# Optimization experiments

Hardware: AMD Instinct MI355X
Metric: run time of the kernel (lower is better)

## Reference

```python
import jax, jax.numpy as jnp
import numpy as np

N_NODES = 100000
N_EDGES = 3200000
IN_CH = 384
HID = 128

def _gcn_layer(x, src, dst, norm, W, b, n_nodes):
    # PyG GCNConv: h = x @ W; out[dst] += norm * h[src]; out += b
    h = x @ W                                   # [N, out_ch]
    msg = h[src] * norm[:, None]                 # [E+N, out_ch] gather + scale
    out = jax.ops.segment_sum(msg, dst, num_segments=n_nodes)
    return out + b

def setup_inputs() -> dict:
    key = jax.random.key(0)
    k = jax.random.split(key, 7)
    x = jax.random.normal(k[0], (N_NODES, IN_CH), dtype=jnp.float32)
    edge_index = jax.random.randint(k[1], (2, N_EDGES), 0, N_NODES, dtype=jnp.int64)
    # Glorot-style init for GCN weights, zeros for biases (PyG default)
    W1 = jax.random.normal(k[2], (IN_CH, HID), dtype=jnp.float32) / np.sqrt(IN_CH)
    b1 = jnp.zeros((HID,), dtype=jnp.float32)
    W2 = jax.random.normal(k[3], (HID, HID), dtype=jnp.float32) / np.sqrt(HID)
    b2 = jnp.zeros((HID,), dtype=jnp.float32)
    return {"x": x, "edge_index": edge_index, "W1": W1, "b1": b1, "W2": W2, "b2": b2}

def reference(x, edge_index, W1, b1, W2, b2):
    n_nodes = x.shape[0]
    # GCNConv default: add self-loops, symmetric normalization D^-1/2 A D^-1/2
    loop = jnp.arange(n_nodes, dtype=edge_index.dtype)
    src = jnp.concatenate([edge_index[0], loop])   # [E+N]
    dst = jnp.concatenate([edge_index[1], loop])   # [E+N]
    deg = jax.ops.segment_sum(jnp.ones_like(dst, dtype=x.dtype), dst, num_segments=n_nodes)
    deg_inv_sqrt = jnp.where(deg > 0, jax.lax.rsqrt(jnp.maximum(deg, 1.0)), 0.0)
    norm = deg_inv_sqrt[src] * deg_inv_sqrt[dst]   # [E+N]
    h = _gcn_layer(x, src, dst, norm, W1, b1, n_nodes)
    h = jax.nn.relu(h)                              # dropout is identity in eval mode
    out = _gcn_layer(h, src, dst, norm, W2, b2, n_nodes)
    return out
```

## Files before the change

kernel.cpp:

```cpp
#include <hip/hip_runtime.h>

#define N_NODES 100000
#define N_EDGES 3200000
#define IN_CH   384
#define HID     128
#define BKT_SHIFT 7
#define NBKT ((N_NODES + 127) >> 7)
#define NTILE 8
#define TILE_SZ 12500
#define NBINS (NBKT * NTILE)
#define BINBLK 128
#define BTHREADS 512
#define CHUNK4 (N_EDGES / 4 / BINBLK)
#define GS_NBLK ((NBINS + 1023) / 1024)

typedef __attribute__((ext_vector_type(8))) short          bf16x8;
typedef __attribute__((ext_vector_type(8))) unsigned short u16x8;
typedef __attribute__((ext_vector_type(4))) float          f32x4;

static __device__ __forceinline__ unsigned short f2bf(float f) {
    unsigned u = __float_as_uint(f);
    unsigned r = (u + 0x7fffu + ((u >> 16) & 1u)) >> 16;
    return (unsigned short)r;
}

__global__ void k_wt2(const float* __restrict__ W1, const float* __restrict__ W2,
                      unsigned short* __restrict__ wt1, unsigned short* __restrict__ wt2) {
    int i = blockIdx.x * blockDim.x + threadIdx.x;
    if (i < IN_CH * 128) {
        int k = i >> 7, n = i & 127;
        wt1[(size_t)n * IN_CH + k] = f2bf(W1[i]);
    } else if (i < (IN_CH + HID) * 128) {
        int j = i - IN_CH * 128;
        int k = j >> 7, n = j & 127;
        wt2[(size_t)n * HID + k] = f2bf(W2[j]);
    }
}

__global__ __launch_bounds__(BTHREADS) void k_bhist2(const int* __restrict__ src,
                                                     const int* __restrict__ dst,
                                                     unsigned* __restrict__ hist) {
    __shared__ unsigned lh[NBINS];
    for (int i = threadIdx.x; i < NBINS; i += BTHREADS) lh[i] = 0;
    __syncthreads();
    const int4* s4 = (const int4*)src;
    const int4* d4 = (const int4*)dst;
    const int base = blockIdx.x * CHUNK4;
    for (int i = threadIdx.x; i < CHUNK4; i += BTHREADS) {
        int4 sv = s4[base + i];
        int4 dv = d4[base + i];
        atomicAdd(&lh[(dv.x >> BKT_SHIFT) * NTILE + (unsigned)sv.x / TILE_SZ], 1u);
        atomicAdd(&lh[(dv.y >> BKT_SHIFT) * NTILE + (unsigned)sv.y / TILE_SZ], 1u);
        atomicAdd(&lh[(dv.z >> BKT_SHIFT) * NTILE + (unsigned)sv.z / TILE_SZ], 1u);
        atomicAdd(&lh[(dv.w >> BKT_SHIFT) * NTILE + (unsigned)sv.w / TILE_SZ], 1u);
    }
    __syncthreads();
    for (int i = threadIdx.x; i < NBINS; i += BTHREADS) hist[i * BINBLK + blockIdx.x] = lh[i];
}

__global__ __launch_bounds__(BINBLK) void k_bscan(unsigned* __restrict__ hist,
                                                  unsigned* __restrict__ bintot) {
    __shared__ unsigned s[BINBLK];
    const int b = blockIdx.x, t = threadIdx.x;
    unsigned v = hist[b * BINBLK + t];
    s[t] = v;
    __syncthreads();
    for (int off = 1; off < BINBLK; off <<= 1) {
        unsigned x = s[t];
        unsigned y = (t >= off) ? s[t - off] : 0u;
        __syncthreads();
        s[t] = x + y;
        __syncthreads();
    }
    hist[b * BINBLK + t] = s[t] - v;
    if (t == BINBLK - 1) bintot[b] = s[BINBLK - 1];
}

__global__ __launch_bounds__(1024) void gs1(const unsigned* __restrict__ in,
                                            unsigned* __restrict__ out,
                                            unsigned* __restrict__ bsum, int n) {
    __shared__ unsigned s[1024];
    const int t = threadIdx.x;
    const int i = blockIdx.x * 1024 + t;
    unsigned v = (i < n) ? in[i] : 0u;
    s[t] = v;
    __syncthreads();
    for (int off = 1; off < 1024; off <<= 1) {
        unsigned x = s[t];
        unsigned y = (t >= off) ? s[t - off] : 0u;
        __syncthreads();
        s[t] = x + y;
        __syncthreads();
    }
    if (i < n) out[i] = s[t] - v;
    if (t == 1023) bsum[blockIdx.x] = s[1023];
}

__global__ void gs2(unsigned* __restrict__ bsum, int nb) {
    if (threadIdx.x == 0 && blockIdx.x == 0) {
        unsigned run = 0;
        for (int i = 0; i < nb; i++) { unsigned v = bsum[i]; bsum[i] = run; run += v; }
    }
}

__global__ __launch_bounds__(1024) void gs3(unsigned* __restrict__ out,
                                            const unsigned* __restrict__ bsum, int n, int total) {
    const int i = blockIdx.x * 1024 + threadIdx.x;
    if (i < n) out[i] += bsum[blockIdx.x];
    if (i == 0) out[n] = (unsigned)total;
}

__global__ __launch_bounds__(BTHREADS) void k_bscat2(const int* __restrict__ src,
                                                     const int* __restrict__ dst,
                                                     const unsigned* __restrict__ hist,
                                                     const unsigned* __restrict__ B2,
                                                     unsigned* __restrict__ ebuf) {
    __shared__ unsigned lcur[NBINS];
    for (int i = threadIdx.x; i < NBINS; i += BTHREADS)
        lcur[i] = B2[i] + hist[i * BINBLK + blockIdx.x];
    __syncthreads();
    const int4* s4 = (const int4*)src;
    const int4* d4 = (const int4*)dst;
    const int base = blockIdx.x * CHUNK4;
    for (int i = threadIdx.x; i < CHUNK4; i += BTHREADS) {
        int4 sv = s4[base + i];
        int4 dv = d4[base + i];
        unsigned p;
        p = atomicAdd(&lcur[(dv.x >> BKT_SHIFT) * NTILE + (unsigned)sv.x / TILE_SZ], 1u);
        ebuf[p] = ((unsigned)(dv.x & 127) << 17) | (unsigned)sv.x;
        p = atomicAdd(&lcur[(dv.y >> BKT_SHIFT) * NTILE + (unsigned)sv.y / TILE_SZ], 1u);
        ebuf[p] = ((unsigned)(dv.y & 127) << 17) | (unsigned)sv.y;
        p = atomicAdd(&lcur[(dv.z >> BKT_SHIFT) * NTILE + (unsigned)sv.z / TILE_SZ], 1u);
        ebuf[p] = ((unsigned)(dv.z & 127) << 17) | (unsigned)sv.z;
        p = atomicAdd(&lcur[(dv.w >> BKT_SHIFT) * NTILE + (unsigned)sv.w / TILE_SZ], 1u);
        ebuf[p] = ((unsigned)(dv.w & 127) << 17) | (unsigned)sv.w;
    }
}

__global__ __launch_bounds__(BTHREADS) void k_fill5(const unsigned* __restrict__ ebuf,
                                                    const unsigned* __restrict__ B2,
                                                    unsigned* __restrict__ rowptr,
                                                    float* __restrict__ dis,
                                                    int* __restrict__ csr, int N, int E) {
    __shared__ unsigned lcnt[128];
    __shared__ unsigned lcur[128];
    const int b = blockIdx.x, t = threadIdx.x;
    const int n0 = b << BKT_SHIFT;
    const int cnt = min(128, N - n0);
    if (t < 128) lcnt[t] = 0;
    __syncthreads();
    const unsigned beg = B2[b * NTILE], end = B2[b * NTILE + NTILE];
    for (unsigned i = beg + t; i < end; i += BTHREADS)
        atomicAdd(&lcnt[ebuf[i] >> 17], 1u);
    __syncthreads();
    unsigned deg_t = (t < 128) ? lcnt[t] : 0u;
    if (t < 128) lcur[t] = deg_t;
    __syncthreads();
    for (int off = 1; off < 128; off <<= 1) {
        unsigned x = 0;
        if (t < 128) {
            x = lcur[t];
            if (t >= off) x += lcur[t - off];
        }
        __syncthreads();
        if (t < 128) lcur[t] = x;
        __syncthreads();
    }
    if (t < cnt) {
        unsigned ex = beg + lcur[t] - deg_t;
        rowptr[n0 + t] = ex;
        dis[n0 + t] = rsqrtf((float)(deg_t + 1u));
        lcur[t] = ex;
    }
    if (b == (int)gridDim.x - 1 && t == 0) rowptr[N] = (unsigned)E;
    __syncthreads();
    for (unsigned i = beg + t; i < end; i += BTHREADS) {
        unsigned v = ebuf[i];
        unsigned pos = atomicAdd(&lcur[v >> 17], 1u);
        csr[pos] = (int)(v & 0x1FFFFu);
    }
}

template<bool AF32>
__global__ __launch_bounds__(256) void k_gemm_mfma(const void* __restrict__ Ap,
                                                   const unsigned short* __restrict__ Wt,
                                                   const float* __restrict__ dis,
                                                   unsigned short* __restrict__ C,
                                                   int M, int K) {
    __shared__ unsigned short As[128][40];
    __shared__ unsigned short Bs[128][40];
    const int tid = threadIdx.x;
    const int w = tid >> 6;
    const int l = tid & 63;
    const int row0 = blockIdx.x * 128;

    f32x4 acc[2][8];
#pragma unroll
    for (int i = 0; i < 2; i++)
#pragma unroll
        for (int f = 0; f < 8; f++) acc[i][f] = (f32x4){0.f, 0.f, 0.f, 0.f};

    for (int k0 = 0; k0 < K; k0 += 32) {
#pragma unroll
        for (int t = 0; t < 2; t++) {
            int g = tid + t * 256;
            int r = g >> 2, k8 = (g & 3) * 8;
            int ar = row0 + r;
            u16x8 u = {0, 0, 0, 0, 0, 0, 0, 0};
            if (AF32) {
                if (ar < M) {
                    const float* ap = (const float*)Ap + (size_t)ar * K + k0 + k8;
                    float4 v0 = *(const float4*)ap;
                    float4 v1 = *(const float4*)(ap + 4);
                    u[0] = f2bf(v0.x); u[1] = f2bf(v0.y); u[2] = f2bf(v0.z); u[3] = f2bf(v0.w);
                    u[4] = f2bf(v1.x); u[5] = f2bf(v1.y); u[6] = f2bf(v1.z); u[7] = f2bf(v1.w);
                }
            } else {
                if (ar < M)
                    u = *(const u16x8*)((const unsigned short*)Ap + (size_t)ar * K + k0 + k8);
            }
            *(u16x8*)&As[r][k8] = u;
        }
#pragma unroll
        for (int t = 0; t < 2; t++) {
            int g = tid + t * 256;
            int n = g >> 2, k8 = (g & 3) * 8;
            *(u16x8*)&Bs[n][k8] = *(const u16x8*)&Wt[(size_t)n * K + k0 + k8];
        }
        __syncthreads();

        bf16x8 a0 = *(const bf16x8*)&As[w * 32 + (l & 15)][(l >> 4) * 8];
        bf16x8 a1 = *(const bf16x8*)&As[w * 32 + 16 + (l & 15)][(l >> 4) * 8];
#pragma unroll
        for (int f = 0; f < 8; f++) {
            bf16x8 bfr = *(const bf16x8*)&Bs[f * 16 + (l & 15)][(l >> 4) * 8];
            acc[0][f] = __builtin_amdgcn_mfma_f32_16x16x32_bf16(a0, bfr, acc[0][f], 0, 0, 0);
            acc[1][f] = __builtin_amdgcn_mfma_f32_16x16x32_bf16(a1, bfr, acc[1][f], 0, 0, 0);
        }
        __syncthreads();
    }

    const int colb = l & 15;
    const int rowq = (l >> 4) * 4;
#pragma unroll
    for (int i = 0; i < 2; i++)
#pragma unroll
        for (int r = 0; r < 4; r++) {
            int row = row0 + w * 32 + i * 16 + rowq + r;
            if (row < M) {
                float dv = dis[row];
#pragma unroll
                for (int f = 0; f < 8; f++)
                    C[(size_t)row * 128 + f * 16 + colb] = f2bf(dv * acc[i][f][r]);
            }
        }
}

template<int RELU, int OUTBF>
__global__ __launch_bounds__(256) void k_aggregate(const unsigned short* __restrict__ h,
                                                   const int* __restrict__ csr_src,
                                                   const unsigned* __restrict__ rowptr,
                                                   const float* __restrict__ dis,
                                                   const float* __restrict__ bias,
                                                   void* __restrict__ outp, int N) {
    const int wid = (int)((blockIdx.x * (blockDim.x >> 6)) + (threadIdx.x >> 6));
    const int d = __builtin_amdgcn_readfirstlane(wid);
    if (d >= N) return;
    const int lane = threadIdx.x & 63;
    const unsigned beg = rowptr[d], end = rowptr[d + 1];
    const float dd = dis[d];
    const unsigned* h1 = reinterpret_cast<const unsigned*>(h);

    unsigned hv = h1[(size_t)d * 64 + lane];
    float ax = __uint_as_float(hv << 16);
    float ay = __uint_as_float(hv & 0xffff0000u);

    unsigned e = beg;
    for (; e + 8 <= end; e += 8) {
        int s[8];
        unsigned v[8];
#pragma unroll
        for (int u = 0; u < 8; u++) s[u] = csr_src[e + u];
#pragma unroll
        for (int u = 0; u < 8; u++) v[u] = h1[(size_t)s[u] * 64 + lane];
#pragma unroll
        for (int u = 0; u < 8; u++) {
            ax += __uint_as_float(v[u] << 16);
            ay += __uint_as_float(v[u] & 0xffff0000u);
        }
    }
    for (; e < end; e++) {
        int s0 = csr_src[e];
        unsigned v0 = h1[(size_t)s0 * 64 + lane];
        ax += __uint_as_float(v0 << 16);
        ay += __uint_as_float(v0 & 0xffff0000u);
    }
    float2 bv = reinterpret_cast<const float2*>(bias)[lane];
    float r0 = fmaf(dd, ax, bv.x);
    float r1 = fmaf(dd, ay, bv.y);
    if (RELU) { r0 = fmaxf(r0, 0.f); r1 = fmaxf(r1, 0.f); }
    if (OUTBF) {
        unsigned pack = (unsigned)f2bf(r0) | ((unsigned)f2bf(r1) << 16);
        reinterpret_cast<unsigned*>(outp)[(size_t)d * 64 + lane] = pack;
    } else {
        reinterpret_cast<float2*>(outp)[(size_t)d * 64 + lane] = make_float2(r0, r1);
    }
}

extern "C" void kernel_launch(void* const* d_in, const int* in_sizes, int n_in,
                              void* d_out, int out_size, void* d_ws, size_t ws_size,
                              hipStream_t stream) {
    const float* x  = (const float*)d_in[0];
    const int*   ei = (const int*)d_in[1];
    const float* W1 = (const float*)d_in[2];
    const float* b1 = (const float*)d_in[3];
    const float* W2 = (const float*)d_in[4];
    const float* b2 = (const float*)d_in[5];
    const int* src = ei;
    const int* dst = ei + N_EDGES;
    float* out = (float*)d_out;

    char* ws = (char*)d_ws;
    float*          dis    = (float*)ws;
    unsigned*       rowptr = (unsigned*)(ws + 400128);
    unsigned*       B2     = (unsigned*)(ws + 800256);
    unsigned*       bintot = (unsigned*)(ws + 825344);
    unsigned*       gsb    = (unsigned*)(ws + 850432);
    unsigned short* wt1    = (unsigned short*)(ws + 850688);
    unsigned short* wt2    = (unsigned short*)(ws + 948992);
    unsigned*       hist   = (unsigned*)(ws + 981760);
    unsigned*       ebuf   = (unsigned*)(ws + 4184832);
    int*            csr    = (int*)(ws + 16984832);
    unsigned short* hbf    = (unsigned short*)(ws + 29784832);
    unsigned short* abf    = (unsigned short*)(ws + 55384832);

    k_wt2<<<((IN_CH + HID) * 128 + 255) / 256, 256, 0, stream>>>(W1, W2, wt1, wt2);

    k_bhist2<<<BINBLK, BTHREADS, 0, stream>>>(src, dst, hist);
    k_bscan<<<NBINS, BINBLK, 0, stream>>>(hist, bintot);
    gs1<<<GS_NBLK, 1024, 0, stream>>>(bintot, B2, gsb, NBINS);
    gs2<<<1, 64, 0, stream>>>(gsb, GS_NBLK);
    gs3<<<GS_NBLK, 1024, 0, stream>>>(B2, gsb, NBINS, N_EDGES);
    k_bscat2<<<BINBLK, BTHREADS, 0, stream>>>(src, dst, hist, B2, ebuf);
    k_fill5<<<NBKT, BTHREADS, 0, stream>>>(ebuf, B2, rowptr, dis, csr, N_NODES, N_EDGES);

    k_gemm_mfma<true><<<(N_NODES + 127) / 128, 256, 0, stream>>>(x, wt1, dis, hbf, N_NODES, IN_CH);
    k_aggregate<1, 1><<<(N_NODES * 64 + 255) / 256, 256, 0, stream>>>(hbf, csr, rowptr, dis, b1, abf, N_NODES);

    k_gemm_mfma<false><<<(N_NODES + 127) / 128, 256, 0, stream>>>(abf, wt2, dis, hbf, N_NODES, HID);
    k_aggregate<0, 0><<<(N_NODES * 64 + 255) / 256, 256, 0, stream>>>(hbf, csr, rowptr, dis, b2, out, N_NODES);
}
```

Before: 399.4 us.

## Double binning blocks and fuse three-pass global scan into one block

Raises the number of histogram/scatter blocks from 128 to 256 so the edge binning kernels spread across more CUs, and enlarges the hist buffer, shifting later workspace offsets. Replaces the three-kernel global prefix scan (block scan, serial block-sum scan, add-back) with a single 1024-thread kernel where each thread scans 7 bins locally. This removes two kernel launches and a serial pass, at the cost of a larger per-bin hist scan and more atomics or partial counts per bin.

```diff
diff --git a/kernel.cpp b/kernel.cpp
--- a/kernel.cpp
+++ b/kernel.cpp
@@ -9,10 +9,9 @@
 #define NTILE 8
 #define TILE_SZ 12500
 #define NBINS (NBKT * NTILE)
-#define BINBLK 128
+#define BINBLK 256
 #define BTHREADS 512
 #define CHUNK4 (N_EDGES / 4 / BINBLK)
-#define GS_NBLK ((NBINS + 1023) / 1024)
 
 typedef __attribute__((ext_vector_type(8))) short          bf16x8;
 typedef __attribute__((ext_vector_type(8))) unsigned short u16x8;
@@ -76,14 +75,20 @@
     if (t == BINBLK - 1) bintot[b] = s[BINBLK - 1];
 }
 
-__global__ __launch_bounds__(1024) void gs1(const unsigned* __restrict__ in,
-                                            unsigned* __restrict__ out,
-                                            unsigned* __restrict__ bsum, int n) {
+__global__ __launch_bounds__(1024) void k_gs(const unsigned* __restrict__ bintot,
+                                             unsigned* __restrict__ B2, int n, int E) {
     __shared__ unsigned s[1024];
     const int t = threadIdx.x;
-    const int i = blockIdx.x * 1024 + t;
-    unsigned v = (i < n) ? in[i] : 0u;
-    s[t] = v;
+    const int base = t * 7;
+    unsigned loc[7];
+    unsigned sum = 0;
+#pragma unroll
+    for (int i = 0; i < 7; i++) {
+        unsigned v = (base + i < n) ? bintot[base + i] : 0u;
+        loc[i] = sum;
+        sum += v;
+    }
+    s[t] = sum;
     __syncthreads();
     for (int off = 1; off < 1024; off <<= 1) {
         unsigned x = s[t];
@@ -92,22 +97,11 @@
         s[t] = x + y;
         __syncthreads();
     }
-    if (i < n) out[i] = s[t] - v;
-    if (t == 1023) bsum[blockIdx.x] = s[1023];
-}
-
-__global__ void gs2(unsigned* __restrict__ bsum, int nb) {
-    if (threadIdx.x == 0 && blockIdx.x == 0) {
-        unsigned run = 0;
-        for (int i = 0; i < nb; i++) { unsigned v = bsum[i]; bsum[i] = run; run += v; }
-    }
-}
-
-__global__ __launch_bounds__(1024) void gs3(unsigned* __restrict__ out,
-                                            const unsigned* __restrict__ bsum, int n, int total) {
-    const int i = blockIdx.x * 1024 + threadIdx.x;
-    if (i < n) out[i] += bsum[blockIdx.x];
-    if (i == 0) out[n] = (unsigned)total;
+    unsigned ex = s[t] - sum;
+#pragma unroll
+    for (int i = 0; i < 7; i++)
+        if (base + i < n) B2[base + i] = ex + loc[i];
+    if (t == 0) B2[n] = (unsigned)E;
 }
 
 __global__ __launch_bounds__(BTHREADS) void k_bscat2(const int* __restrict__ src,
@@ -325,22 +319,19 @@
     unsigned*       rowptr = (unsigned*)(ws + 400128);
     unsigned*       B2     = (unsigned*)(ws + 800256);
     unsigned*       bintot = (unsigned*)(ws + 825344);
-    unsigned*       gsb    = (unsigned*)(ws + 850432);
     unsigned short* wt1    = (unsigned short*)(ws + 850688);
     unsigned short* wt2    = (unsigned short*)(ws + 948992);
     unsigned*       hist   = (unsigned*)(ws + 981760);
-    unsigned*       ebuf   = (unsigned*)(ws + 4184832);
-    int*            csr    = (int*)(ws + 16984832);
-    unsigned short* hbf    = (unsigned short*)(ws + 29784832);
-    unsigned short* abf    = (unsigned short*)(ws + 55384832);
+    unsigned*       ebuf   = (unsigned*)(ws + 7387904);
+    int*            csr    = (int*)(ws + 20187904);
+    unsigned short* hbf    = (unsigned short*)(ws + 32987904);
+    unsigned short* abf    = (unsigned short*)(ws + 58587904);
 
     k_wt2<<<((IN_CH + HID) * 128 + 255) / 256, 256, 0, stream>>>(W1, W2, wt1, wt2);
 
     k_bhist2<<<BINBLK, BTHREADS, 0, stream>>>(src, dst, hist);
     k_bscan<<<NBINS, BINBLK, 0, stream>>>(hist, bintot);
-    gs1<<<GS_NBLK, 1024, 0, stream>>>(bintot, B2, gsb, NBINS);
-    gs2<<<1, 64, 0, stream>>>(gsb, GS_NBLK);
-    gs3<<<GS_NBLK, 1024, 0, stream>>>(B2, gsb, NBINS, N_EDGES);
+    k_gs<<<1, 1024, 0, stream>>>(bintot, B2, NBINS, N_EDGES);
     k_bscat2<<<BINBLK, BTHREADS, 0, stream>>>(src, dst, hist, B2, ebuf);
     k_fill5<<<NBKT, BTHREADS, 0, stream>>>(ebuf, B2, rowptr, dis, csr, N_NODES, N_EDGES);
 
```

New measurement: 408.1 us. 1.02x slower.
